# Kernel optimization log

Hardware: AMD Instinct MI355X
Metric: run time of the kernel (lower is better)

## Reference

```python
import jax, jax.numpy as jnp
import numpy as np

HIDDEN = 1024
N_HEADS = 16
HEAD_DIM = 64
BS, QS = 4, 2048
NEG = -60000.0


def setup_inputs() -> dict:
    key = jax.random.key(0)
    k1, k2, k3, k4 = jax.random.split(key, 4)
    x = jax.random.normal(k1, (BS, QS, HIDDEN), dtype=jnp.float32)
    att_mask = jax.random.randint(k2, (BS, QS, QS), 0, 2).astype(bool)
    # nn.Linear(hidden, out, bias=False): store as [in, out] so y = x @ W
    W_qk = jax.random.normal(k3, (HIDDEN, 2 * N_HEADS * HEAD_DIM), dtype=jnp.float32) / np.sqrt(HIDDEN)
    W_v = jax.random.normal(k4, (HIDDEN, N_HEADS), dtype=jnp.float32) / np.sqrt(HIDDEN)
    return {"x": x, "att_mask": att_mask, "W_qk": W_qk, "W_v": W_v}


def reference(x, att_mask, W_qk, W_v):
    # mem is None -> c = x, ks == qs
    bs, qs, _ = x.shape
    n_heads = W_v.shape[1]
    head_dim = W_qk.shape[1] // (2 * n_heads)
    att_scale = 1.0 / head_dim ** 0.5

    qk = x @ W_qk                                   # [b, k, 2*n*d]
    query, key = jnp.split(qk, 2, axis=-1)
    value = x @ W_v                                 # [b, k, n]  (per-head V dim is 1)

    q = query.reshape(bs, qs, n_heads, head_dim)
    k = key.reshape(bs, qs, n_heads, head_dim)

    # att_score: [b, q, k, n]
    scores = jnp.einsum('bqnd,bknd->bqkn', q, k) * att_scale
    scores = jnp.where(att_mask[..., None], NEG, scores)  # True = masked
    prob = jax.nn.softmax(scores, axis=2)           # softmax over k
    # attended bqnd with d=1, then .sum(2) over heads -> [b, q, 1]
    attended = jnp.einsum('bqkn,bkn->bqn', prob, value)
    out = attended.sum(-1, keepdims=True)           # [b, q, 1]

    padded_mask = att_mask[:, -1]                   # [b, k] == [b, q]
    out = jnp.where(padded_mask[..., None], NEG, out)
    out = jax.nn.sigmoid(out)
    # torch version also returns out.nonzero() (data-dependent shape); omitted for jit.
    return out
```

## Files before the change

kernel.cpp:

```cpp
#include <hip/hip_runtime.h>

typedef unsigned short u16;
typedef unsigned int u32;
typedef unsigned long long u64;
typedef __attribute__((ext_vector_type(8))) short bf16x8;
typedef __attribute__((ext_vector_type(4))) float f32x4;

#define BATCH 4
#define SEQ 2048
#define HID 1024
#define NHEAD 16
#define HDIM 64
#define C1 0.18033688011112042f

#if __has_builtin(__builtin_amdgcn_exp2f)
#define EXP2(x) __builtin_amdgcn_exp2f(x)
#else
#define EXP2(x) exp2f(x)
#endif

__device__ __forceinline__ u16 f2bf(float f) {
    u32 u = __builtin_bit_cast(u32, f);
    u += 0x7fffu + ((u >> 16) & 1u);
    return (u16)(u >> 16);
}

__device__ __forceinline__ void gl_lds16(const void* g, void* l) {
    __builtin_amdgcn_global_load_lds((const __attribute__((address_space(1))) u32*)g,
                                     (__attribute__((address_space(3))) u32*)l, 16, 0, 0);
}

__global__ __launch_bounds__(256) void front(const float* __restrict__ x,
                                             const float* __restrict__ Wv,
                                             const float* __restrict__ W,
                                             const unsigned char* __restrict__ mask,
                                             u16* __restrict__ xb,
                                             float* __restrict__ vT,
                                             u16* __restrict__ wT,
                                             int* __restrict__ flag) {
    __shared__ __align__(16) float smem[16 * 1024];
    int bid = blockIdx.x;
    if (bid < 512) {
        float* xs = smem;
        int s0 = bid * 16;
        const float4* xg = (const float4*)(x + (size_t)s0 * HID);
        float4* xd = (float4*)xs;
        ushort4* xo = (ushort4*)(xb + (size_t)s0 * HID);
#pragma unroll
        for (int j = 0; j < 16; ++j) {
            int i = j * 256 + threadIdx.x;
            float4 v = xg[i];
            xd[i] = v;
            ushort4 o;
            o.x = f2bf(v.x); o.y = f2bf(v.y); o.z = f2bf(v.z); o.w = f2bf(v.w);
            xo[i] = o;
        }
        __syncthreads();
        int sl = threadIdx.x >> 4, n = threadIdx.x & 15;
        const float4* xrow = (const float4*)&xs[sl * HID];
        float acc = 0.f;
        for (int h4 = 0; h4 < 256; ++h4) {
            float4 xv = xrow[h4];
            acc += xv.x * Wv[(h4 * 4 + 0) * 16 + n] + xv.y * Wv[(h4 * 4 + 1) * 16 + n]
                 + xv.z * Wv[(h4 * 4 + 2) * 16 + n] + xv.w * Wv[(h4 * 4 + 3) * 16 + n];
        }
        int s = s0 + sl;
        int b = s >> 11, q = s & 2047;
        vT[((size_t)b * 16 + n) * SEQ + q] = acc;
    } else if (bid < 2560) {
        float (*t)[33] = (float (*)[33])smem;
        int tb = bid - 512;
        int nb = tb & 63, hb = tb >> 6;
        int tx = threadIdx.x & 31, ty = threadIdx.x >> 5;
#pragma unroll
        for (int i = 0; i < 4; ++i)
            t[ty + i * 8][tx] = W[(size_t)(hb * 32 + ty + i * 8) * 2048 + nb * 32 + tx];
        __syncthreads();
#pragma unroll
        for (int i = 0; i < 4; ++i)
            wT[(size_t)(nb * 32 + ty + i * 8) * 1024 + hb * 32 + tx] = f2bf(t[tx][ty + i * 8]);
    } else {
        int* any = (int*)smem;
        if (threadIdx.x == 0) *any = 0;
        __syncthreads();
        const uint4* m4 = (const uint4*)mask;
        u32 acc = 0;
#pragma unroll
        for (int j = 0; j < 16; ++j) {
            uint4 v = m4[threadIdx.x + j * 256];
            acc |= (v.x | v.y | v.z | v.w) & 0xFFFFFF00u;
        }
        if (acc) atomicOr(any, 1);
        __syncthreads();
        if (threadIdx.x == 0) *flag = (*any == 0) ? 1 : 0;
    }
}

__global__ void bitpack(const void* __restrict__ mask, const int* __restrict__ flag,
                        u64* __restrict__ bm) {
    int base = blockIdx.x * 2048 + threadIdx.x;
    int fl = *flag;
#pragma unroll
    for (int k = 0; k < 8; ++k) {
        int i = base + k * 256;
        int v;
        if (fl) v = ((const int*)mask)[i];
        else    v = ((const unsigned char*)mask)[i];
        u64 bits = __ballot(v == 0);
        if ((threadIdx.x & 63) == 0) bm[i >> 6] = bits;
    }
}

__global__ __launch_bounds__(256) void proj_gemm(const u16* __restrict__ xb,
                                                 const u16* __restrict__ wT,
                                                 u16* __restrict__ qkb) {
    __shared__ __align__(16) u16 As[2][128 * 64];
    __shared__ __align__(16) u16 Bs[2][128 * 64];
    int tid = threadIdx.x, w = tid >> 6, lane = tid & 63;
    int g = lane >> 4, l15 = lane & 15;
    int bid = blockIdx.x;
    int swz = (bid & 7) * 128 + (bid >> 3);
    int bm = swz >> 4, bn = swz & 15;
    int m0 = bm * 128, n0 = bn * 128;
    int wm = w >> 1, wn = w & 1;
    const u16* asrc[4];
    const u16* bsrc[4];
#pragma unroll
    for (int j = 0; j < 4; ++j) {
        int ci = (w * 4 + j) * 64 + lane;
        int row = ci >> 3, cl = (ci & 7) ^ (row & 7);
        asrc[j] = xb + (size_t)(m0 + row) * HID + cl * 8;
        bsrc[j] = wT + (size_t)(n0 + row) * HID + cl * 8;
    }
    f32x4 acc[4][4] = {};
#pragma unroll
    for (int j = 0; j < 4; ++j) {
        gl_lds16(asrc[j], &As[0][(w * 4 + j) * 512]);
        gl_lds16(bsrc[j], &Bs[0][(w * 4 + j) * 512]);
        asrc[j] += 64; bsrc[j] += 64;
    }
    for (int kt = 0; kt < 16; ++kt) {
        int cur = kt & 1;
        asm volatile("s_waitcnt vmcnt(0)" ::: "memory");
        __builtin_amdgcn_s_barrier();
        __builtin_amdgcn_sched_barrier(0);
        if (kt < 15) {
#pragma unroll
            for (int j = 0; j < 4; ++j) {
                gl_lds16(asrc[j], &As[cur ^ 1][(w * 4 + j) * 512]);
                gl_lds16(bsrc[j], &Bs[cur ^ 1][(w * 4 + j) * 512]);
                asrc[j] += 64; bsrc[j] += 64;
            }
        }
#pragma unroll
        for (int kk = 0; kk < 2; ++kk) {
            bf16x8 af[4], bf[4];
#pragma unroll
            for (int m = 0; m < 4; ++m) {
                int row = wm * 64 + m * 16 + l15;
                int cp = (kk * 4 + g) ^ (row & 7);
                af[m] = *(const bf16x8*)&As[cur][row * 64 + cp * 8];
            }
#pragma unroll
            for (int n = 0; n < 4; ++n) {
                int row = wn * 64 + n * 16 + l15;
                int cp = (kk * 4 + g) ^ (row & 7);
                bf[n] = *(const bf16x8*)&Bs[cur][row * 64 + cp * 8];
            }
#pragma unroll
            for (int m = 0; m < 4; ++m)
#pragma unroll
                for (int n = 0; n < 4; ++n)
                    acc[m][n] = __builtin_amdgcn_mfma_f32_16x16x32_bf16(af[m], bf[n], acc[m][n], 0, 0, 0);
        }
    }
    float scale = (bn < 8) ? C1 : 1.0f;
#pragma unroll
    for (int m = 0; m < 4; ++m)
#pragma unroll
        for (int n = 0; n < 4; ++n)
#pragma unroll
            for (int r = 0; r < 4; ++r) {
                int row = m0 + wm * 64 + m * 16 + g * 4 + r;
                int col = n0 + wn * 64 + n * 16 + l15;
                qkb[(size_t)row * 2048 + col] = f2bf(acc[m][n][r] * scale);
            }
}

__global__ __launch_bounds__(512, 4) void attn(const u16* __restrict__ qkb,
                                               const float* __restrict__ vT,
                                               const u64* __restrict__ bmk,
                                               float* __restrict__ hatt) {
    __shared__ __align__(16) u16 Ks[3][64 * 64];
    __shared__ __align__(16) float Vh[2048];
    __shared__ __align__(16) float Tb[16][4];
    int tid = threadIdx.x, w = tid >> 6, lane = tid & 63;
    int g = lane >> 4, l15 = lane & 15, g4 = g * 4;
    int bid = blockIdx.x;
    int swzb = (bid & 7) * 64 + (bid >> 3);
    int qt = swzb & 7, h = (swzb >> 3) & 15, b = swzb >> 7;
    int q0 = qt * 256;
    if (tid < 64) Tb[tid >> 2][tid & 3] = (float)(((tid >> 2) >> (tid & 3)) & 1);
    int qA = q0 + w * 32 + l15, qB = qA + 16;
    const u16* qrowA = qkb + (size_t)(b * SEQ + qA) * 2048 + h * 64;
    const u16* qrowB = qkb + (size_t)(b * SEQ + qB) * 2048 + h * 64;
    bf16x8 qfA0 = *(const bf16x8*)(qrowA + g * 8);
    bf16x8 qfA1 = *(const bf16x8*)(qrowA + 32 + g * 8);
    bf16x8 qfB0 = *(const bf16x8*)(qrowB + g * 8);
    bf16x8 qfB1 = *(const bf16x8*)(qrowB + 32 + g * 8);
    gl_lds16(vT + ((size_t)b * 16 + h) * SEQ + tid * 4, &Vh[w * 256]);
    const u64* mrowA = bmk + ((size_t)b * SEQ + qA) * 32;
    const u64* mrowB = bmk + ((size_t)b * SEQ + qB) * 32;
    int srow = tid >> 3, scol = (tid & 7) ^ (srow & 7);
    const u16* ksrc = qkb + (size_t)(b * SEQ + srow) * 2048 + 1024 + h * 64 + scol * 8;
    u64 mA_cur = mrowA[0], mB_cur = mrowB[0];
    gl_lds16(ksrc, &Ks[0][w * 512]); ksrc += 64 * 2048;
    u64 mA_nxt = mrowA[1], mB_nxt = mrowB[1];
    gl_lds16(ksrc, &Ks[1][w * 512]); ksrc += 64 * 2048;
    int e0[4], e1[4];
#pragma unroll
    for (int cb = 0; cb < 4; ++cb) {
        int krow = cb * 16 + l15;
        e0[cb] = krow * 64 + ((g) ^ (krow & 7)) * 8;
        e1[cb] = krow * 64 + ((4 + g) ^ (krow & 7)) * 8;
    }
    float nmA0 = 0.f, nmA1 = 0.f, nmA2 = 0.f, nmA3 = 0.f;
    float dnA0 = 0.f, dnA1 = 0.f, dnA2 = 0.f, dnA3 = 0.f;
    float nmB0 = 0.f, nmB1 = 0.f, nmB2 = 0.f, nmB3 = 0.f;
    float dnB0 = 0.f, dnB1 = 0.f, dnB2 = 0.f, dnB3 = 0.f;
    asm volatile("s_waitcnt lgkmcnt(0)" ::: "memory");

    auto compute = [&](int kt) {
        const u16* kcur = &Ks[kt % 3][0];
        const float* vk = &Vh[kt * 64 + g4];
        u64 shA = mA_cur >> g4, shB = mB_cur >> g4;
        u32 aLo = (u32)shA, aHi = (u32)(shA >> 32);
        u32 bLo = (u32)shB, bHi = (u32)(shB >> 32);
        int idxA[4] = {(int)(aLo & 15), (int)((aLo >> 16) & 15),
                       (int)(aHi & 15), (int)((aHi >> 16) & 15)};
        int idxB[4] = {(int)(bLo & 15), (int)((bLo >> 16) & 15),
                       (int)(bHi & 15), (int)((bHi >> 16) & 15)};
        __builtin_amdgcn_s_setprio(1);
#pragma unroll
        for (int cb = 0; cb < 4; ++cb) {
            bf16x8 kf0 = *(const bf16x8*)&kcur[e0[cb]];
            bf16x8 kf1 = *(const bf16x8*)&kcur[e1[cb]];
            f32x4 aA = {0.f, 0.f, 0.f, 0.f}, aB = {0.f, 0.f, 0.f, 0.f};
            aA = __builtin_amdgcn_mfma_f32_16x16x32_bf16(kf0, qfA0, aA, 0, 0, 0);
            aA = __builtin_amdgcn_mfma_f32_16x16x32_bf16(kf1, qfA1, aA, 0, 0, 0);
            aB = __builtin_amdgcn_mfma_f32_16x16x32_bf16(kf0, qfB0, aB, 0, 0, 0);
            aB = __builtin_amdgcn_mfma_f32_16x16x32_bf16(kf1, qfB1, aB, 0, 0, 0);
            const float4 mA4 = *(const float4*)&Tb[idxA[cb]][0];
            const float4 mB4 = *(const float4*)&Tb[idxB[cb]][0];
            const float4 vv = *(const float4*)&vk[cb * 16];
            float pA0 = EXP2(aA[0]) * mA4.x, pA1 = EXP2(aA[1]) * mA4.y;
            float pA2 = EXP2(aA[2]) * mA4.z, pA3 = EXP2(aA[3]) * mA4.w;
            float pB0 = EXP2(aB[0]) * mB4.x, pB1 = EXP2(aB[1]) * mB4.y;
            float pB2 = EXP2(aB[2]) * mB4.z, pB3 = EXP2(aB[3]) * mB4.w;
            dnA0 += pA0; dnA1 += pA1; dnA2 += pA2; dnA3 += pA3;
            dnB0 += pB0; dnB1 += pB1; dnB2 += pB2; dnB3 += pB3;
            nmA0 = fmaf(pA0, vv.x, nmA0); nmA1 = fmaf(pA1, vv.y, nmA1);
            nmA2 = fmaf(pA2, vv.z, nmA2); nmA3 = fmaf(pA3, vv.w, nmA3);
            nmB0 = fmaf(pB0, vv.x, nmB0); nmB1 = fmaf(pB1, vv.y, nmB1);
            nmB2 = fmaf(pB2, vv.z, nmB2); nmB3 = fmaf(pB3, vv.w, nmB3);
        }
        __builtin_amdgcn_s_setprio(0);
    };

    for (int kt = 0; kt < 31; ++kt) {
        asm volatile("s_waitcnt vmcnt(3)" ::: "memory");
        __builtin_amdgcn_s_barrier();
        __builtin_amdgcn_sched_barrier(0);
        u64 mA_n2, mB_n2;
        if (kt < 30) {
            mA_n2 = mrowA[kt + 2]; mB_n2 = mrowB[kt + 2];
            gl_lds16(ksrc, &Ks[(kt + 2) % 3][w * 512]); ksrc += 64 * 2048;
        } else { mA_n2 = 0; mB_n2 = 0; }
        compute(kt);
        mA_cur = mA_nxt; mB_cur = mB_nxt;
        mA_nxt = mA_n2; mB_nxt = mB_n2;
    }
    asm volatile("s_waitcnt vmcnt(0)" ::: "memory");
    __builtin_amdgcn_s_barrier();
    __builtin_amdgcn_sched_barrier(0);
    compute(31);

    float numA = (nmA0 + nmA1) + (nmA2 + nmA3);
    float denA = (dnA0 + dnA1) + (dnA2 + dnA3);
    float numB = (nmB0 + nmB1) + (nmB2 + nmB3);
    float denB = (dnB0 + dnB1) + (dnB2 + dnB3);
    numA += __shfl_xor(numA, 16); denA += __shfl_xor(denA, 16);
    numA += __shfl_xor(numA, 32); denA += __shfl_xor(denA, 32);
    numB += __shfl_xor(numB, 16); denB += __shfl_xor(denB, 16);
    numB += __shfl_xor(numB, 32); denB += __shfl_xor(denB, 32);
    if (g == 0) {
        hatt[((size_t)b * SEQ + qA) * 16 + h] = numA / denA;
        hatt[((size_t)b * SEQ + qB) * 16 + h] = numB / denB;
    }
}

__global__ void epi(const float* __restrict__ hatt, const void* __restrict__ mask,
                    const int* __restrict__ flag, float* __restrict__ out) {
    int i = blockIdx.x * 256 + threadIdx.x;
    int b = i >> 11, q = i & 2047;
    const float4* hp = (const float4*)(hatt + (size_t)i * 16);
    float t = 0.f;
#pragma unroll
    for (int j = 0; j < 4; ++j) {
        float4 u = hp[j];
        t += u.x + u.y + u.z + u.w;
    }
    size_t mi = ((size_t)b * SEQ + (SEQ - 1)) * SEQ + q;
    int m;
    if (*flag) m = ((const int*)mask)[mi];
    else       m = ((const unsigned char*)mask)[mi];
    out[i] = m ? 0.f : 1.f / (1.f + expf(-t));
}

extern "C" void kernel_launch(void* const* d_in, const int* in_sizes, int n_in,
                              void* d_out, int out_size, void* d_ws, size_t ws_size,
                              hipStream_t stream) {
    const float* x = (const float*)d_in[0];
    const void* mask = d_in[1];
    const float* Wqk = (const float*)d_in[2];
    const float* Wv = (const float*)d_in[3];
    float* out = (float*)d_out;
    char* ws = (char*)d_ws;
    u16* xb = (u16*)(ws + 0);
    u16* wT = (u16*)(ws + 16777216);
    u16* qkb = (u16*)(ws + 20971520);
    float* vT = (float*)(ws + 54525952);
    u64* bm = (u64*)(ws + 55050240);
    float* hatt = (float*)(ws + 0);
    int* flag = (int*)(ws + 57147392);

    front<<<2561, 256, 0, stream>>>(x, Wv, Wqk, (const unsigned char*)mask,
                                    xb, vT, wT, flag);
    bitpack<<<8192, 256, 0, stream>>>(mask, flag, bm);
    proj_gemm<<<1024, 256, 0, stream>>>(xb, wT, qkb);
    attn<<<512, 512, 0, stream>>>(qkb, vT, bm, hatt);
    epi<<<32, 256, 0, stream>>>(hatt, mask, flag, out);
}
```

Baseline: 154.3 us.

## Fold mask bitpack into front kernel and pair K tiles in attention pipeline

Merges the bitpack kernel into the front kernel as extra blocks, with each block working out the mask dtype flag locally from the first 4KB of the mask. This removes one launch and the dependency on the global flag. The attention kernel moves from a triple-buffered, one-tile-per-barrier K pipeline to double buffering with two 64-row K tiles per stage, which halves the number of barriers. It also drops the s_setprio hints. The trade-off is a full vmcnt(0) wait each stage, which gives less load/compute overlap, plus repeated flag detection in every bitpack block.

```diff
diff --git a/kernel.cpp b/kernel.cpp
--- a/kernel.cpp
+++ b/kernel.cpp
@@ -37,7 +37,8 @@
                                              u16* __restrict__ xb,
                                              float* __restrict__ vT,
                                              u16* __restrict__ wT,
-                                             int* __restrict__ flag) {
+                                             int* __restrict__ flag,
+                                             u64* __restrict__ bm) {
     __shared__ __align__(16) float smem[16 * 1024];
     int bid = blockIdx.x;
     if (bid < 512) {
@@ -79,7 +80,7 @@
 #pragma unroll
         for (int i = 0; i < 4; ++i)
             wT[(size_t)(nb * 32 + ty + i * 8) * 1024 + hb * 32 + tx] = f2bf(t[tx][ty + i * 8]);
-    } else {
+    } else if (bid == 2560) {
         int* any = (int*)smem;
         if (threadIdx.x == 0) *any = 0;
         __syncthreads();
@@ -93,21 +94,24 @@
         if (acc) atomicOr(any, 1);
         __syncthreads();
         if (threadIdx.x == 0) *flag = (*any == 0) ? 1 : 0;
-    }
-}
-
-__global__ void bitpack(const void* __restrict__ mask, const int* __restrict__ flag,
-                        u64* __restrict__ bm) {
-    int base = blockIdx.x * 2048 + threadIdx.x;
-    int fl = *flag;
-#pragma unroll
-    for (int k = 0; k < 8; ++k) {
-        int i = base + k * 256;
-        int v;
-        if (fl) v = ((const int*)mask)[i];
-        else    v = ((const unsigned char*)mask)[i];
-        u64 bits = __ballot(v == 0);
-        if ((threadIdx.x & 63) == 0) bm[i >> 6] = bits;
+    } else {
+        int* sflag = (int*)smem;
+        if (threadIdx.x == 0) *sflag = 0;
+        __syncthreads();
+        uint4 pv = ((const uint4*)mask)[threadIdx.x];
+        if ((pv.x | pv.y | pv.z | pv.w) & 0xFFFFFF00u) atomicOr(sflag, 1);
+        __syncthreads();
+        int fl = (*sflag == 0) ? 1 : 0;
+        int base = (bid - 2561) * 2048 + threadIdx.x;
+#pragma unroll
+        for (int k = 0; k < 8; ++k) {
+            int i = base + k * 256;
+            int v;
+            if (fl) v = ((const int*)mask)[i];
+            else    v = ((const unsigned char*)mask)[i];
+            u64 bits = __ballot(v == 0);
+            if ((threadIdx.x & 63) == 0) bm[i >> 6] = bits;
+        }
     }
 }
 
@@ -191,7 +195,7 @@
                                                const float* __restrict__ vT,
                                                const u64* __restrict__ bmk,
                                                float* __restrict__ hatt) {
-    __shared__ __align__(16) u16 Ks[3][64 * 64];
+    __shared__ __align__(16) u16 Ks[2][2][64 * 64];
     __shared__ __align__(16) float Vh[2048];
     __shared__ __align__(16) float Tb[16][4];
     int tid = threadIdx.x, w = tid >> 6, lane = tid & 63;
@@ -213,10 +217,9 @@
     const u64* mrowB = bmk + ((size_t)b * SEQ + qB) * 32;
     int srow = tid >> 3, scol = (tid & 7) ^ (srow & 7);
     const u16* ksrc = qkb + (size_t)(b * SEQ + srow) * 2048 + 1024 + h * 64 + scol * 8;
-    u64 mA_cur = mrowA[0], mB_cur = mrowB[0];
-    gl_lds16(ksrc, &Ks[0][w * 512]); ksrc += 64 * 2048;
-    u64 mA_nxt = mrowA[1], mB_nxt = mrowB[1];
-    gl_lds16(ksrc, &Ks[1][w * 512]); ksrc += 64 * 2048;
+    u64 mA0 = mrowA[0], mA1 = mrowA[1], mB0 = mrowB[0], mB1 = mrowB[1];
+    gl_lds16(ksrc, &Ks[0][0][w * 512]); ksrc += 64 * 2048;
+    gl_lds16(ksrc, &Ks[0][1][w * 512]); ksrc += 64 * 2048;
     int e0[4], e1[4];
 #pragma unroll
     for (int cb = 0; cb < 4; ++cb) {
@@ -228,19 +231,18 @@
     float dnA0 = 0.f, dnA1 = 0.f, dnA2 = 0.f, dnA3 = 0.f;
     float nmB0 = 0.f, nmB1 = 0.f, nmB2 = 0.f, nmB3 = 0.f;
     float dnB0 = 0.f, dnB1 = 0.f, dnB2 = 0.f, dnB3 = 0.f;
-    asm volatile("s_waitcnt lgkmcnt(0)" ::: "memory");
-
-    auto compute = [&](int kt) {
-        const u16* kcur = &Ks[kt % 3][0];
+    asm volatile("s_waitcnt vmcnt(0) lgkmcnt(0)" ::: "memory");
+    __builtin_amdgcn_s_barrier();
+
+    auto compute = [&](int kt, const u16* kcur, u64 mwA, u64 mwB) {
         const float* vk = &Vh[kt * 64 + g4];
-        u64 shA = mA_cur >> g4, shB = mB_cur >> g4;
+        u64 shA = mwA >> g4, shB = mwB >> g4;
         u32 aLo = (u32)shA, aHi = (u32)(shA >> 32);
         u32 bLo = (u32)shB, bHi = (u32)(shB >> 32);
         int idxA[4] = {(int)(aLo & 15), (int)((aLo >> 16) & 15),
                        (int)(aHi & 15), (int)((aHi >> 16) & 15)};
         int idxB[4] = {(int)(bLo & 15), (int)((bLo >> 16) & 15),
                        (int)(bHi & 15), (int)((bHi >> 16) & 15)};
-        __builtin_amdgcn_s_setprio(1);
 #pragma unroll
         for (int cb = 0; cb < 4; ++cb) {
             bf16x8 kf0 = *(const bf16x8*)&kcur[e0[cb]];
@@ -264,26 +266,23 @@
             nmB0 = fmaf(pB0, vv.x, nmB0); nmB1 = fmaf(pB1, vv.y, nmB1);
             nmB2 = fmaf(pB2, vv.z, nmB2); nmB3 = fmaf(pB3, vv.w, nmB3);
         }
-        __builtin_amdgcn_s_setprio(0);
     };
 
-    for (int kt = 0; kt < 31; ++kt) {
-        asm volatile("s_waitcnt vmcnt(3)" ::: "memory");
+    for (int p = 0; p < 16; ++p) {
+        asm volatile("s_waitcnt vmcnt(0)" ::: "memory");
         __builtin_amdgcn_s_barrier();
         __builtin_amdgcn_sched_barrier(0);
-        u64 mA_n2, mB_n2;
-        if (kt < 30) {
-            mA_n2 = mrowA[kt + 2]; mB_n2 = mrowB[kt + 2];
-            gl_lds16(ksrc, &Ks[(kt + 2) % 3][w * 512]); ksrc += 64 * 2048;
-        } else { mA_n2 = 0; mB_n2 = 0; }
-        compute(kt);
-        mA_cur = mA_nxt; mB_cur = mB_nxt;
-        mA_nxt = mA_n2; mB_nxt = mB_n2;
-    }
-    asm volatile("s_waitcnt vmcnt(0)" ::: "memory");
-    __builtin_amdgcn_s_barrier();
-    __builtin_amdgcn_sched_barrier(0);
-    compute(31);
+        u64 nA0 = 0, nA1 = 0, nB0 = 0, nB1 = 0;
+        if (p < 15) {
+            gl_lds16(ksrc, &Ks[(p + 1) & 1][0][w * 512]); ksrc += 64 * 2048;
+            gl_lds16(ksrc, &Ks[(p + 1) & 1][1][w * 512]); ksrc += 64 * 2048;
+            nA0 = mrowA[2 * p + 2]; nA1 = mrowA[2 * p + 3];
+            nB0 = mrowB[2 * p + 2]; nB1 = mrowB[2 * p + 3];
+        }
+        compute(2 * p,     &Ks[p & 1][0][0], mA0, mB0);
+        compute(2 * p + 1, &Ks[p & 1][1][0], mA1, mB1);
+        mA0 = nA0; mA1 = nA1; mB0 = nB0; mB1 = nB1;
+    }
 
     float numA = (nmA0 + nmA1) + (nmA2 + nmA3);
     float denA = (dnA0 + dnA1) + (dnA2 + dnA3);
@@ -334,9 +333,8 @@
     float* hatt = (float*)(ws + 0);
     int* flag = (int*)(ws + 57147392);
 
-    front<<<2561, 256, 0, stream>>>(x, Wv, Wqk, (const unsigned char*)mask,
-                                    xb, vT, wT, flag);
-    bitpack<<<8192, 256, 0, stream>>>(mask, flag, bm);
+    front<<<10753, 256, 0, stream>>>(x, Wv, Wqk, (const unsigned char*)mask,
+                                     xb, vT, wT, flag, bm);
     proj_gemm<<<1024, 256, 0, stream>>>(xb, wT, qkb);
     attn<<<512, 512, 0, stream>>>(qkb, vT, bm, hatt);
     epi<<<32, 256, 0, stream>>>(hatt, mask, flag, out);
```

Result: slower. 183.9 us (+19.2%).
